# Optimization experiments

Measured on AMD Instinct MI355X. Metric: run time of the kernel, lower is better.

## Reference

```python
import jax, jax.numpy as jnp
import numpy as np

B, S, NFT, K1, K2, NOUT = 2048, 512, 64, 16, 12, 32


def setup_inputs() -> dict:
    key = jax.random.key(0)
    ks = jax.random.split(key, 8)
    X = jax.random.normal(ks[0], (B, S, NFT), dtype=jnp.float32)
    setSizes = jax.random.randint(ks[1], (B,), 0, S, dtype=jnp.int32)
    W1 = jax.random.normal(ks[2], (NFT, K1), dtype=jnp.float32) / np.sqrt(NFT)
    b1 = jnp.zeros((K1,), dtype=jnp.float32)
    W2 = jax.random.normal(ks[3], (K1, K2), dtype=jnp.float32) / np.sqrt(K1)
    b2 = jnp.zeros((K2,), dtype=jnp.float32)
    W3 = jax.random.normal(ks[4], (K2, NOUT), dtype=jnp.float32) / np.sqrt(K2)
    b3 = jnp.zeros((NOUT,), dtype=jnp.float32)
    return {"X": X, "setSizes": setSizes, "W1": W1, "b1": b1,
            "W2": W2, "b2": b2, "W3": W3, "b3": b3}


def reference(X, setSizes, W1, b1, W2, b2, W3, b3):
    # per-element MLP: [B,S,nft] -> [B,S,k2]
    h = jax.nn.relu(jnp.einsum('bsf,fk->bsk', X, W1) + b1)
    h = jnp.einsum('bsk,kj->bsj', h, W2) + b2
    # masked sum-pool over set dim (replaces the per-batch zero-padding loop)
    mask = (jnp.arange(S)[None, :] < setSizes[:, None])  # [B,S]
    pooled = jnp.sum(jnp.where(mask[:, :, None], h, 0.0), axis=1)  # [B,k2]
    return pooled @ W3 + b3  # [B,nout]
```

## Files before the change

kernel.cpp:

```cpp
#include <hip/hip_runtime.h>

#define B_    2048
#define S_    512
#define NFT_  64
#define K1_   16
#define K2_   12
#define NOUT_ 32
#define ROWS_PER_BLK 128
#define CHUNKS 4
#define XPAD 68

__global__ __launch_bounds__(256) void k1_embed_pool(
    const float* __restrict__ X, const int* __restrict__ setSizes,
    const float* __restrict__ W1, const float* __restrict__ b1,
    float* __restrict__ part)
{
    __shared__ __align__(16) float xs[ROWS_PER_BLK][XPAD];
    __shared__ float red[4][K1_];

    const int t    = threadIdx.x;
    const int blk  = blockIdx.x;
    const int b    = blk >> 2;
    const int s0   = (blk & 3) * ROWS_PER_BLK;
    const int wave = t >> 6;
    const int lane = t & 63;
    const int g    = lane >> 4;
    const int k    = lane & 15;

    int n = setSizes[b];
    int n_local = n - s0;
    n_local = n_local < 0 ? 0 : (n_local > ROWS_PER_BLK ? ROWS_PER_BLK : n_local);

    float w[NFT_];
    #pragma unroll
    for (int f = 0; f < NFT_; ++f) w[f] = W1[f * K1_ + k];
    const float bk = b1[k];

    {
        const float4* X4 = (const float4*)X + ((size_t)b * S_ + s0) * (NFT_ / 4);
        const int lim = n_local * (NFT_ / 4);
        #pragma unroll
        for (int i = 0; i < 8; ++i) {
            int idx = t + 256 * i;
            if (idx < lim) {
                float4 v = X4[idx];
                *(float4*)&xs[idx >> 4][(idx & 15) * 4] = v;
            }
        }
    }
    __syncthreads();

    float pool = 0.f;
    const int base = wave * 32;
    int m = n_local - base;
    m = m < 0 ? 0 : (m > 32 ? 32 : m);
    const int steps = (m + 3) >> 2;
    for (int s = 0; s < steps; ++s) {
        const int r = base + s * 4 + g;
        float acc = bk;
        #pragma unroll
        for (int j = 0; j < 16; ++j) {
            float4 x4 = *(const float4*)&xs[r][4 * j];
            acc += x4.x * w[4*j+0] + x4.y * w[4*j+1]
                 + x4.z * w[4*j+2] + x4.w * w[4*j+3];
        }
        if (s * 4 + g < m) pool += (acc > 0.f ? acc : 0.f);
    }

    pool += __shfl_xor(pool, 16, 64);
    pool += __shfl_xor(pool, 32, 64);
    if (lane < K1_) red[wave][lane] = pool;
    __syncthreads();
    if (t < K1_)
        part[(size_t)blk * K1_ + t] = red[0][t] + red[1][t] + red[2][t] + red[3][t];
}

__global__ __launch_bounds__(256) void k2_out(
    const int* __restrict__ setSizes,
    const float* __restrict__ W2, const float* __restrict__ b2,
    const float* __restrict__ W3, const float* __restrict__ b3,
    const float* __restrict__ part, float* __restrict__ out)
{
    __shared__ float w23[K1_ * NOUT_];
    __shared__ float bb[NOUT_];
    const int t = threadIdx.x;

    for (int e = t; e < K1_ * NOUT_; e += 256) {
        int k = e >> 5, o = e & 31;
        float s = 0.f;
        #pragma unroll
        for (int j = 0; j < K2_; ++j) s += W2[k * K2_ + j] * W3[j * NOUT_ + o];
        w23[e] = s;
    }
    if (t < NOUT_) {
        float s = 0.f;
        #pragma unroll
        for (int j = 0; j < K2_; ++j) s += b2[j] * W3[j * NOUT_ + t];
        bb[t] = s;
    }
    __syncthreads();

    const int gid = blockIdx.x * 256 + t;
    const int b = gid >> 5, o = gid & 31;
    const float* p0 = part + (size_t)b * CHUNKS * K1_;
    float r = 0.f;
    #pragma unroll
    for (int k = 0; k < K1_; ++k) {
        float pk = p0[k] + p0[K1_ + k] + p0[2 * K1_ + k] + p0[3 * K1_ + k];
        r += pk * w23[k * NOUT_ + o];
    }
    out[gid] = r + (float)setSizes[b] * bb[o] + b3[o];
}

extern "C" void kernel_launch(void* const* d_in, const int* in_sizes, int n_in,
                              void* d_out, int out_size, void* d_ws, size_t ws_size,
                              hipStream_t stream) {
    const float* X        = (const float*)d_in[0];
    const int*   setSizes = (const int*)  d_in[1];
    const float* W1       = (const float*)d_in[2];
    const float* b1       = (const float*)d_in[3];
    const float* W2       = (const float*)d_in[4];
    const float* b2       = (const float*)d_in[5];
    const float* W3       = (const float*)d_in[6];
    const float* b3       = (const float*)d_in[7];
    float* out  = (float*)d_out;
    float* part = (float*)d_ws;

    hipLaunchKernelGGL(k1_embed_pool, dim3(B_ * CHUNKS), dim3(256), 0, stream,
                       X, setSizes, W1, b1, part);
    hipLaunchKernelGGL(k2_out, dim3(B_ * NOUT_ / 256), dim3(256), 0, stream,
                       setSizes, W2, b2, W3, b3, part, out);
}
```

Before: 380.8 us.

## Fuse embed, pool and output into one kernel using bf16 MFMA

Replaces the two-kernel scalar FP32 pipeline with one kernel per batch element. The first layer now runs on bf16 MFMA 16x16x32 instructions, with X converted to bf16 in registers and read directly from global memory instead of staged through LDS. The W2·W3 output projection is done in the same block, which removes the partial-sum workspace and the second launch. The costs are lower precision from bf16 rounding and fewer blocks (2048 instead of 8192), which may reduce latency hiding for a memory-bound load.

```diff
diff --git a/kernel.cpp b/kernel.cpp
--- a/kernel.cpp
+++ b/kernel.cpp
@@ -6,110 +6,95 @@
 #define K1_   16
 #define K2_   12
 #define NOUT_ 32
-#define ROWS_PER_BLK 128
-#define CHUNKS 4
-#define XPAD 68
 
-__global__ __launch_bounds__(256) void k1_embed_pool(
+typedef __attribute__((ext_vector_type(8))) short bf16x8;
+typedef __attribute__((ext_vector_type(4))) float f32x4;
+
+static __device__ __forceinline__ short f2bf(float x) {
+    union { float f; unsigned u; } v; v.f = x;
+    unsigned r = v.u + 0x7FFF + ((v.u >> 16) & 1);
+    return (short)(r >> 16);
+}
+
+__global__ __launch_bounds__(256) void setembed_fused(
     const float* __restrict__ X, const int* __restrict__ setSizes,
     const float* __restrict__ W1, const float* __restrict__ b1,
-    float* __restrict__ part)
+    const float* __restrict__ W2, const float* __restrict__ b2,
+    const float* __restrict__ W3, const float* __restrict__ b3,
+    float* __restrict__ out)
 {
-    __shared__ __align__(16) float xs[ROWS_PER_BLK][XPAD];
     __shared__ float red[4][K1_];
 
     const int t    = threadIdx.x;
-    const int blk  = blockIdx.x;
-    const int b    = blk >> 2;
-    const int s0   = (blk & 3) * ROWS_PER_BLK;
+    const int b    = blockIdx.x;
     const int wave = t >> 6;
     const int lane = t & 63;
-    const int g    = lane >> 4;
-    const int k    = lane & 15;
+    const int m    = lane & 15;
+    const int quad = lane >> 4;
 
-    int n = setSizes[b];
-    int n_local = n - s0;
-    n_local = n_local < 0 ? 0 : (n_local > ROWS_PER_BLK ? ROWS_PER_BLK : n_local);
+    const int n = setSizes[b];
 
-    float w[NFT_];
+    bf16x8 wf0, wf1;
     #pragma unroll
-    for (int f = 0; f < NFT_; ++f) w[f] = W1[f * K1_ + k];
-    const float bk = b1[k];
-
-    {
-        const float4* X4 = (const float4*)X + ((size_t)b * S_ + s0) * (NFT_ / 4);
-        const int lim = n_local * (NFT_ / 4);
-        #pragma unroll
-        for (int i = 0; i < 8; ++i) {
-            int idx = t + 256 * i;
-            if (idx < lim) {
-                float4 v = X4[idx];
-                *(float4*)&xs[idx >> 4][(idx & 15) * 4] = v;
-            }
-        }
+    for (int j = 0; j < 8; ++j) {
+        wf0[j] = f2bf(W1[(     quad * 8 + j) * K1_ + m]);
+        wf1[j] = f2bf(W1[(32 + quad * 8 + j) * K1_ + m]);
     }
-    __syncthreads();
+    const float bk = b1[m];
 
     float pool = 0.f;
-    const int base = wave * 32;
-    int m = n_local - base;
-    m = m < 0 ? 0 : (m > 32 ? 32 : m);
-    const int steps = (m + 3) >> 2;
-    for (int s = 0; s < steps; ++s) {
-        const int r = base + s * 4 + g;
-        float acc = bk;
+    const int ntiles = (n + 15) >> 4;
+    const float* Xb = X + (size_t)b * S_ * NFT_;
+
+    for (int tl = wave; tl < ntiles; tl += 4) {
+        const int r0 = tl * 16;
+        const float* rowp = Xb + (size_t)(r0 + m) * NFT_ + quad * 8;
+        float4 p0 = *(const float4*)(rowp);
+        float4 p1 = *(const float4*)(rowp + 4);
+        float4 p2 = *(const float4*)(rowp + 32);
+        float4 p3 = *(const float4*)(rowp + 36);
+
+        bf16x8 a0, a1;
+        a0[0] = f2bf(p0.x); a0[1] = f2bf(p0.y); a0[2] = f2bf(p0.z); a0[3] = f2bf(p0.w);
+        a0[4] = f2bf(p1.x); a0[5] = f2bf(p1.y); a0[6] = f2bf(p1.z); a0[7] = f2bf(p1.w);
+        a1[0] = f2bf(p2.x); a1[1] = f2bf(p2.y); a1[2] = f2bf(p2.z); a1[3] = f2bf(p2.w);
+        a1[4] = f2bf(p3.x); a1[5] = f2bf(p3.y); a1[6] = f2bf(p3.z); a1[7] = f2bf(p3.w);
+
+        f32x4 c = {0.f, 0.f, 0.f, 0.f};
+        c = __builtin_amdgcn_mfma_f32_16x16x32_bf16(a0, wf0, c, 0, 0, 0);
+        c = __builtin_amdgcn_mfma_f32_16x16x32_bf16(a1, wf1, c, 0, 0, 0);
+
         #pragma unroll
-        for (int j = 0; j < 16; ++j) {
-            float4 x4 = *(const float4*)&xs[r][4 * j];
-            acc += x4.x * w[4*j+0] + x4.y * w[4*j+1]
-                 + x4.z * w[4*j+2] + x4.w * w[4*j+3];
+        for (int i = 0; i < 4; ++i) {
+            float h = c[i] + bk;
+            h = h > 0.f ? h : 0.f;
+            int row = r0 + quad * 4 + i;
+            pool += (row < n) ? h : 0.f;
         }
-        if (s * 4 + g < m) pool += (acc > 0.f ? acc : 0.f);
     }
 
     pool += __shfl_xor(pool, 16, 64);
     pool += __shfl_xor(pool, 32, 64);
     if (lane < K1_) red[wave][lane] = pool;
     __syncthreads();
-    if (t < K1_)
-        part[(size_t)blk * K1_ + t] = red[0][t] + red[1][t] + red[2][t] + red[3][t];
-}
 
-__global__ __launch_bounds__(256) void k2_out(
-    const int* __restrict__ setSizes,
-    const float* __restrict__ W2, const float* __restrict__ b2,
-    const float* __restrict__ W3, const float* __restrict__ b3,
-    const float* __restrict__ part, float* __restrict__ out)
-{
-    __shared__ float w23[K1_ * NOUT_];
-    __shared__ float bb[NOUT_];
-    const int t = threadIdx.x;
-
-    for (int e = t; e < K1_ * NOUT_; e += 256) {
-        int k = e >> 5, o = e & 31;
-        float s = 0.f;
+    if (t < NOUT_) {
+        const int o = t;
+        float r = 0.f;
         #pragma unroll
-        for (int j = 0; j < K2_; ++j) s += W2[k * K2_ + j] * W3[j * NOUT_ + o];
-        w23[e] = s;
+        for (int k = 0; k < K1_; ++k) {
+            float pk = red[0][k] + red[1][k] + red[2][k] + red[3][k];
+            float w23 = 0.f;
+            #pragma unroll
+            for (int j = 0; j < K2_; ++j)
+                w23 += W2[k * K2_ + j] * W3[j * NOUT_ + o];
+            r += pk * w23;
+        }
+        float bbo = 0.f;
+        #pragma unroll
+        for (int j = 0; j < K2_; ++j) bbo += b2[j] * W3[j * NOUT_ + o];
+        out[(size_t)b * NOUT_ + o] = r + (float)n * bbo + b3[o];
     }
-    if (t < NOUT_) {
-        float s = 0.f;
-        #pragma unroll
-        for (int j = 0; j < K2_; ++j) s += b2[j] * W3[j * NOUT_ + t];
-        bb[t] = s;
-    }
-    __syncthreads();
-
-    const int gid = blockIdx.x * 256 + t;
-    const int b = gid >> 5, o = gid & 31;
-    const float* p0 = part + (size_t)b * CHUNKS * K1_;
-    float r = 0.f;
-    #pragma unroll
-    for (int k = 0; k < K1_; ++k) {
-        float pk = p0[k] + p0[K1_ + k] + p0[2 * K1_ + k] + p0[3 * K1_ + k];
-        r += pk * w23[k * NOUT_ + o];
-    }
-    out[gid] = r + (float)setSizes[b] * bb[o] + b3[o];
 }
 
 extern "C" void kernel_launch(void* const* d_in, const int* in_sizes, int n_in,
@@ -123,11 +108,8 @@
     const float* b2       = (const float*)d_in[5];
     const float* W3       = (const float*)d_in[6];
     const float* b3       = (const float*)d_in[7];
-    float* out  = (float*)d_out;
-    float* part = (float*)d_ws;
+    float* out = (float*)d_out;
 
-    hipLaunchKernelGGL(k1_embed_pool, dim3(B_ * CHUNKS), dim3(256), 0, stream,
-                       X, setSizes, W1, b1, part);
-    hipLaunchKernelGGL(k2_out, dim3(B_ * NOUT_ / 256), dim3(256), 0, stream,
-                       setSizes, W2, b2, W3, b3, part, out);
+    hipLaunchKernelGGL(setembed_fused, dim3(B_), dim3(256), 0, stream,
+                       X, setSizes, W1, b1, W2, b2, W3, b3, out);
 }
```

Measured after the change: 343.9 us. 1.11x faster.
